# Kernel tuning notes

Measured on AMD Instinct MI355X. Metric: run time of the kernel, lower is better.

Reference implementation:

```python
import jax, jax.numpy as jnp
import numpy as np

H = 64        # hidden_dim
A = 21        # N_ACTIONS
B = 262144    # batch size


def setup_inputs() -> dict:
    key = jax.random.key(0)
    ks = jax.random.split(key, 32)

    def w(k, shape):
        fan_in = shape[0]
        return (jax.random.normal(k, shape, jnp.float32) / np.float32(np.sqrt(fan_in)))

    inp = {
        "x": jax.random.normal(ks[0], (B, 2, 2), jnp.float32),
        "b_act1": jax.random.randint(ks[1], (B,), 0, A),
        "b_act2": jax.random.randint(ks[2], (B,), 0, A),
        # enc: Linear(2,H), ReLU, Linear(H,H), ReLU
        "enc_w1": w(ks[3], (2, H)), "enc_b1": jnp.zeros((H,), jnp.float32),
        "enc_w2": w(ks[4], (H, H)), "enc_b2": jnp.zeros((H,), jnp.float32),
        # q_net: Linear(H,H), ReLU, Linear(H,A)
        "q_w1": w(ks[5], (H, H)), "q_b1": jnp.zeros((H,), jnp.float32),
        "q_w2": w(ks[6], (H, A)), "q_b2": jnp.zeros((A,), jnp.float32),
        # v_net: Linear(H,H), ReLU, Linear(H,1)
        "v_w1": w(ks[7], (H, H)), "v_b1": jnp.zeros((H,), jnp.float32),
        "v_w2": w(ks[8], (H, 1)), "v_b2": jnp.zeros((1,), jnp.float32),
        # lin2: Linear(H+A,H), ReLU, Linear(H,H), ReLU, Linear(H,H)
        "l2_w1": w(ks[9], (H + A, H)), "l2_b1": jnp.zeros((H,), jnp.float32),
        "l2_w2": w(ks[10], (H, H)), "l2_b2": jnp.zeros((H,), jnp.float32),
        "l2_w3": w(ks[11], (H, H)), "l2_b3": jnp.zeros((H,), jnp.float32),
        # lin3, lin4
        "l3_w": w(ks[12], (H, H)), "l3_b": jnp.zeros((H,), jnp.float32),
        "l4_w": w(ks[13], (H, A)), "l4_b": jnp.zeros((A,), jnp.float32),
        # q_prime_net: Linear(H,2H) ELU Linear(2H,H) ELU Linear(H,H) ELU Linear(H,1)
        "qp_w1": w(ks[14], (H, 2 * H)), "qp_b1": jnp.zeros((2 * H,), jnp.float32),
        "qp_w2": w(ks[15], (2 * H, H)), "qp_b2": jnp.zeros((H,), jnp.float32),
        "qp_w3": w(ks[16], (H, H)), "qp_b3": jnp.zeros((H,), jnp.float32),
        "qp_w4": w(ks[17], (H, 1)), "qp_b4": jnp.zeros((1,), jnp.float32),
    }
    return inp


def reference(x, b_act1, b_act2,
              enc_w1, enc_b1, enc_w2, enc_b2,
              q_w1, q_b1, q_w2, q_b2,
              v_w1, v_b1, v_w2, v_b2,
              l2_w1, l2_b1, l2_w2, l2_b2, l2_w3, l2_b3,
              l3_w, l3_b, l4_w, l4_b,
              qp_w1, qp_b1, qp_w2, qp_b2, qp_w3, qp_b3, qp_w4, qp_b4):
    relu = jax.nn.relu
    elu = jax.nn.elu

    def enc(z):
        return relu(relu(z @ enc_w1 + enc_b1) @ enc_w2 + enc_b2)

    def q_net(h):
        return relu(h @ q_w1 + q_b1) @ q_w2 + q_b2

    def lin2(e):  # ends with bare Linear (no final activation)
        h = relu(e @ l2_w1 + l2_b1)
        h = relu(h @ l2_w2 + l2_b2)
        return h @ l2_w3 + l2_b3

    def q_prime(z):
        h = elu(z @ qp_w1 + qp_b1)
        h = elu(h @ qp_w2 + qp_b2)
        h = elu(h @ qp_w3 + qp_b3)
        return h @ qp_w4 + qp_b4

    h1 = enc(x[:, 0, :])  # [B,H]
    h2 = enc(x[:, 1, :])
    q1, q2 = q_net(h1), q_net(h2)              # [B,A]
    key2 = jnp.stack([h1, h2], axis=1)          # [B,2,H]
    vtot = relu((h1 + h2) @ v_w1 + v_b1) @ v_w2 + v_b2  # [B,1]

    def joint(act1, act2):
        oh1 = jax.nn.one_hot(act1, A, dtype=h1.dtype)
        oh2 = jax.nn.one_hot(act2, A, dtype=h2.dtype)
        e = jnp.stack([jnp.concatenate([h1, oh1], axis=-1),
                       jnp.concatenate([h2, oh2], axis=-1)], axis=1)  # [B,2,H+A]
        key1 = lin2(e)                              # [B,2,H]
        q = q_prime(key1.mean(axis=1))              # [B,1]
        return key1, q

    key1, joint_qs = joint(b_act1, b_act2)
    a1_max = jnp.argmax(q1, axis=1)
    a2_max = jnp.argmax(q2, axis=1)
    key1_max, joint_max_qs = joint(a1_max, a2_max)

    def q_jt(k1):
        z = key2 + k1.mean(axis=1, keepdims=True) - k1 / 2  # [B,2,H]
        return relu(z @ l3_w + l3_b) @ l4_w + l4_b           # [B,2,A]

    q_jt_alt = q_jt(key1)
    q_jt_max_alt = q_jt(key1_max)

    return (q1, q2, joint_qs, joint_max_qs, vtot, q_jt_alt, q_jt_max_alt)
```

## Files before the change

kernel.cpp:

```cpp
#include <hip/hip_runtime.h>
#include <hip/hip_bf16.h>


#define B_TOT 262144

typedef __bf16 bf16_t;
typedef __bf16 bf16x4 __attribute__((ext_vector_type(4)));
typedef __bf16 bf16x8 __attribute__((ext_vector_type(8)));
typedef float  f32x2  __attribute__((ext_vector_type(2)));
typedef float  f32x4  __attribute__((ext_vector_type(4)));

#define MFMA16(a, b, c) __builtin_amdgcn_mfma_f32_16x16x32_bf16((a), (b), (c), 0, 0, 0)

enum : int {
  OFF_VW1  = 0,
  OFF_L2W1 = 4096,
  OFF_L2W2 = 8192,
  OFF_L2W3 = 12288,
  OFF_L3W  = 16384,
  OFF_L4W  = 20480,
  OFF_QP1  = 22528,
  OFF_QP2  = 30720,
  OFF_QP3  = 38912,
  WS_ELEMS = 43008
};
#define WS_BYTES (WS_ELEMS * 2)

enum : int {
  O_Q1   = 0,
  O_Q2   = 21 * B_TOT,
  O_JQ   = 42 * B_TOT,
  O_JMQ  = 43 * B_TOT,
  O_VT   = 44 * B_TOT,
  O_QJT  = 45 * B_TOT,
  O_QJTM = 87 * B_TOT
};

struct RDesc { const float* src; int K; int N; int NT; int off; };
struct RPack { RDesc d[9]; };

__global__ void repack_kernel(RPack P, bf16_t* __restrict__ ws) {
  RDesc d = P.d[blockIdx.x];
  int n = (d.K >> 5) * d.NT * 512;
  for (int i = threadIdx.x; i < n; i += blockDim.x) {
    int j  = i & 7;
    int l  = (i >> 3) & 63;
    int t  = i >> 9;
    int nt = t % d.NT;
    int kc = t / d.NT;
    int sk = kc * 32 + 16 * (j >> 2) + 4 * (l >> 4) + (j & 3);
    int sn = nt * 16 + (l & 15);
    float v = (sn < d.N) ? d.src[sk * d.N + sn] : 0.0f;
    ws[d.off + i] = (bf16_t)v;
  }
}

struct Args {
  const float* x; const int* a1; const int* a2;
  const float* ew1; const float* eb1; const float* ew2; const float* eb2;
  const float* qw1; const float* qb1; const float* qw2; const float* qb2;
  const float* vw1; const float* vb1; const float* vw2; const float* vb2;
  const float* l2w1; const float* l2b1; const float* l2w2; const float* l2b2;
  const float* l2w3; const float* l2b3;
  const float* l3w;  const float* l3b;  const float* l4w;  const float* l4b;
  const float* qpw1; const float* qpb1; const float* qpw2; const float* qpb2;
  const float* qpw3; const float* qpb3; const float* qpw4; const float* qpb4;
  float* out; const bf16_t* ws;
};

struct __align__(16) SMem {
  unsigned char scr[16896];
  bf16_t h1b[64 * 68];
  bf16_t h2b[64 * 68];
  float  bias[768];
  int    acts[128];
  int    amax[128];
  float  red[64][4];
  int    redi[64][4];
};

__device__ __forceinline__ float eluf(float x) {
  return x > 0.f ? x : __expf(x) - 1.0f;
}

__device__ __forceinline__ void fcA64ip(float* __restrict__ f,
                                        const float* __restrict__ W,
                                        const float* __restrict__ Bv,
                                        bf16_t* __restrict__ hb, int r, int g) {
  f32x2 acc[8];
  const f32x2* Bv2 = (const f32x2*)(Bv + g * 16);
#pragma unroll
  for (int i = 0; i < 8; i++) acc[i] = Bv2[i];
  const f32x2* fr = (const f32x2*)(f + r * 66);
#pragma unroll 1
  for (int hh = 0; hh < 2; hh++) {
    f32x2 in[16];
#pragma unroll
    for (int i = 0; i < 16; i++) in[i] = fr[16 * hh + i];
#pragma unroll 4
    for (int k2 = 0; k2 < 16; k2++) {
      int k = 32 * hh + 2 * k2;
      const f32x2* wr0 = (const f32x2*)(W + k * 64 + g * 16);
      const f32x2* wr1 = (const f32x2*)(W + (k + 1) * 64 + g * 16);
      f32x2 a0 = {in[k2][0], in[k2][0]};
      f32x2 a1 = {in[k2][1], in[k2][1]};
#pragma unroll
      for (int i = 0; i < 8; i++) acc[i] += a0 * wr0[i];
#pragma unroll
      for (int i = 0; i < 8; i++) acc[i] += a1 * wr1[i];
    }
  }
  __syncthreads();
#pragma unroll
  for (int i = 0; i < 8; i++) {
    float v0 = fmaxf(acc[i][0], 0.f), v1 = fmaxf(acc[i][1], 0.f);
    f32x2 v = {v0, v1};
    *(f32x2*)(f + r * 66 + g * 16 + 2 * i) = v;
    if (hb) {
      hb[r * 68 + g * 16 + 2 * i]     = (bf16_t)v0;
      hb[r * 68 + g * 16 + 2 * i + 1] = (bf16_t)v1;
    }
  }
  __syncthreads();
}

template <int NC>
__device__ __forceinline__ void qn2(const float* __restrict__ fin, const float* __restrict__ W21,
                                    const float* __restrict__ Bv, float* __restrict__ qo,
                                    int r, int colbase, float& bv, int& bi) {
  float acc[NC];
#pragma unroll
  for (int i = 0; i < NC; i++) acc[i] = Bv[colbase + i];
  for (int k2 = 0; k2 < 32; k2++) {
    f32x2 a = *(const f32x2*)(fin + r * 66 + 2 * k2);
    const float* wr0 = W21 + (2 * k2) * 21 + colbase;
    const float* wr1 = W21 + (2 * k2 + 1) * 21 + colbase;
#pragma unroll
    for (int i = 0; i < NC; i++) acc[i] = fmaf(a[0], wr0[i], acc[i]);
#pragma unroll
    for (int i = 0; i < NC; i++) acc[i] = fmaf(a[1], wr1[i], acc[i]);
  }
  bv = -3e38f; bi = 0;
#pragma unroll
  for (int i = 0; i < NC; i++) {
    qo[i] = acc[i];
    if (acc[i] > bv) { bv = acc[i]; bi = colbase + i; }
  }
}

template <bool USEWS, int NT, int KC>
__device__ __forceinline__ f32x4 tileT(const bf16x8* __restrict__ WF,
                                       const float* __restrict__ Wp, int N, int woff,
                                       const bf16x8* __restrict__ bin,
                                       const float* __restrict__ bias, int bbase,
                                       int nt, int l, int c, int u) {
  f32x4 a = *(const f32x4*)(bias + bbase + nt * 16 + 4 * u);
#pragma unroll
  for (int kc = 0; kc < KC; kc++) {
    bf16x8 w;
    if constexpr (USEWS) {
      w = WF[(woff >> 3) + (kc * NT + nt) * 64 + l];
    } else {
      int sn = nt * 16 + c;
      if (sn < N) {
#pragma unroll
        for (int j = 0; j < 8; j++)
          w[j] = (bf16_t)Wp[(kc * 32 + 16 * (j >> 2) + 4 * u + (j & 3)) * N + sn];
      } else {
#pragma unroll
        for (int j = 0; j < 8; j++) w[j] = (bf16_t)0.0f;
      }
    }
    a = MFMA16(w, bin[kc], a);
  }
  return a;
}

template <int MODE>
__device__ __forceinline__ bf16x8 pack2(f32x4 t0, f32x4 t1) {
  bf16x8 r;
#pragma unroll
  for (int j = 0; j < 8; j++) {
    float v = (j >> 2) ? t1[j & 3] : t0[j & 3];
    if constexpr (MODE == 1) v = fmaxf(v, 0.f);
    if constexpr (MODE == 2) v = eluf(v);
    r[j] = (bf16_t)v;
  }
  return r;
}

template <bool USEWS>
__global__ __launch_bounds__(256, 2) void qtran_main(Args A) {
  __shared__ SMem sm;
  const int t = threadIdx.x;
  const int wgbase = blockIdx.x * 64;
  const int r = t & 63;
  const int g = __builtin_amdgcn_readfirstlane(t >> 6);

  float* f0 = (float*)sm.scr;

  if (t < 64) {
    sm.bias[t]        = A.vb1[t];
    sm.bias[64 + t]   = A.l2b1[t];
    sm.bias[128 + t]  = A.l2b2[t];
    sm.bias[192 + t]  = A.l2b3[t];
    sm.bias[384 + t]  = A.qpb2[t];
    sm.bias[448 + t]  = A.qpb3[t];
    sm.bias[512 + t]  = A.l3b[t];
    sm.bias[608 + t]  = A.vw2[t];
    sm.bias[672 + t]  = A.qpw4[t];
    sm.acts[t]        = A.a1[wgbase + t];
    sm.acts[64 + t]   = A.a2[wgbase + t];
  } else if (t < 192) {
    sm.bias[256 + t - 64] = A.qpb1[t - 64];
  } else if (t < 224) {
    int i = t - 192;
    sm.bias[576 + i] = (i < 21) ? A.l4b[i] : 0.0f;
  } else if (t == 224) {
    sm.bias[736] = A.vb2[0];
    sm.bias[737] = A.qpb4[0];
  }

  const int rowg = wgbase + r;
  float4 xv = ((const float4*)A.x)[rowg];
#pragma unroll 1
  for (int s = 0; s < 2; ++s) {
    float xa = s ? xv.z : xv.x;
    float xb = s ? xv.w : xv.y;
#pragma unroll
    for (int cc = 0; cc < 16; cc += 2) {
      int col = g * 16 + cc;
      float h0 = fmaf(xa, A.ew1[col],     fmaf(xb, A.ew1[64 + col],     A.eb1[col]));
      float h1 = fmaf(xa, A.ew1[col + 1], fmaf(xb, A.ew1[64 + col + 1], A.eb1[col + 1]));
      f32x2 v = {fmaxf(h0, 0.f), fmaxf(h1, 0.f)};
      *(f32x2*)(f0 + r * 66 + col) = v;
    }
    __syncthreads();
    fcA64ip(f0, A.ew2, A.eb2, s ? sm.h2b : sm.h1b, r, g);
    fcA64ip(f0, A.qw1, A.qb1, nullptr, r, g);
    {
      float* qo = A.out + (s ? O_Q2 : O_Q1) + rowg * 21;
      float bv; int bi;
      if (g == 0)      qn2<6>(f0, A.qw2, A.qb2, qo,      r, 0,  bv, bi);
      else if (g == 1) qn2<5>(f0, A.qw2, A.qb2, qo + 6,  r, 6,  bv, bi);
      else if (g == 2) qn2<5>(f0, A.qw2, A.qb2, qo + 11, r, 11, bv, bi);
      else             qn2<5>(f0, A.qw2, A.qb2, qo + 16, r, 16, bv, bi);
      sm.red[r][g] = bv; sm.redi[r][g] = bi;
    }
    __syncthreads();
    if (t < 64) {
      float b0 = sm.red[t][0]; int i0 = sm.redi[t][0];
#pragma unroll
      for (int grp = 1; grp < 4; grp++)
        if (sm.red[t][grp] > b0) { b0 = sm.red[t][grp]; i0 = sm.redi[t][grp]; }
      sm.amax[s * 64 + t] = i0;
    }
    __syncthreads();
  }

  const int l = t & 63;
  const int c = l & 15, u = l >> 4;
  const int rb = g * 16;
  const int row = rb + c;
  float* out = A.out;
  const bf16x8* WF = (const bf16x8*)A.ws;
  const float* bias = sm.bias;
  float* S = (float*)sm.scr;

  auto HG = [&](const bf16_t* __restrict__ HB, int kc) -> bf16x8 {
    const bf16_t* p = HB + row * 68 + kc * 32 + 4 * u;
    bf16x4 lo = *(const bf16x4*)p;
    bf16x4 hi = *(const bf16x4*)(p + 16);
    bf16x8 rr;
#pragma unroll
    for (int d = 0; d < 4; d++) { rr[d] = lo[d]; rr[4 + d] = hi[d]; }
    return rr;
  };

  {
    bf16x8 aS[2];
#pragma unroll
    for (int kc = 0; kc < 2; kc++) {
      bf16x8 a1 = HG(sm.h1b, kc), a2 = HG(sm.h2b, kc);
      bf16x8 s8;
#pragma unroll
      for (int i = 0; i < 8; i++) s8[i] = (bf16_t)((float)a1[i] + (float)a2[i]);
      aS[kc] = s8;
    }
    float pr = 0.f;
#pragma unroll
    for (int nt = 0; nt < 4; nt++) {
      f32x4 tv = tileT<USEWS, 4, 2>(WF, A.vw1, 64, OFF_VW1, aS, bias, 0, nt, l, c, u);
      f32x4 wv = *(const f32x4*)(bias + 608 + nt * 16 + 4 * u);
#pragma unroll
      for (int p = 0; p < 4; p++) pr += fmaxf(tv[p], 0.f) * wv[p];
    }
    pr += __shfl_xor(pr, 16, 64);
    pr += __shfl_xor(pr, 32, 64);
    if (u == 0) out[O_VT + wgbase + row] = pr + bias[736];
  }

  auto J = [&](const int* __restrict__ asrc, int jointBase, int qjtBase) {
    bf16x8 k1f[2][2];
#pragma unroll
    for (int j = 0; j < 2; j++) {
      const bf16_t* HB = j ? sm.h2b : sm.h1b;
      const int act = asrc[j * 64 + row];
      bf16x8 bh[2];
#pragma unroll
      for (int kc = 0; kc < 2; kc++) bh[kc] = HG(HB, kc);
      const float* ohp = A.l2w1 + (64 + act) * 64 + 4 * u;
      bf16x8 b1[2];
#pragma unroll
      for (int f = 0; f < 2; f++) {
        f32x4 t0 = tileT<USEWS, 4, 2>(WF, A.l2w1, 64, OFF_L2W1, bh, bias, 64, 2 * f, l, c, u);
        f32x4 t1 = tileT<USEWS, 4, 2>(WF, A.l2w1, 64, OFF_L2W1, bh, bias, 64, 2 * f + 1, l, c, u);
        t0 += *(const f32x4*)(ohp + (2 * f) * 16);
        t1 += *(const f32x4*)(ohp + (2 * f + 1) * 16);
        b1[f] = pack2<1>(t0, t1);
      }
      bf16x8 b2[2];
#pragma unroll
      for (int f = 0; f < 2; f++) {
        f32x4 t0 = tileT<USEWS, 4, 2>(WF, A.l2w2, 64, OFF_L2W2, b1, bias, 128, 2 * f, l, c, u);
        f32x4 t1 = tileT<USEWS, 4, 2>(WF, A.l2w2, 64, OFF_L2W2, b1, bias, 128, 2 * f + 1, l, c, u);
        b2[f] = pack2<1>(t0, t1);
      }
#pragma unroll
      for (int f = 0; f < 2; f++) {
        f32x4 t0 = tileT<USEWS, 4, 2>(WF, A.l2w3, 64, OFF_L2W3, b2, bias, 192, 2 * f, l, c, u);
        f32x4 t1 = tileT<USEWS, 4, 2>(WF, A.l2w3, 64, OFF_L2W3, b2, bias, 192, 2 * f + 1, l, c, u);
        k1f[j][f] = pack2<0>(t0, t1);
      }
    }
#pragma unroll
    for (int j = 0; j < 2; j++) {
      const bf16_t* HB = j ? sm.h2b : sm.h1b;
      bf16x8 aZ[2];
#pragma unroll
      for (int kc = 0; kc < 2; kc++) {
        bf16x8 h8 = HG(HB, kc);
        bf16x8 kk = k1f[1 - j][kc];
#pragma unroll
        for (int i = 0; i < 8; i++)
          aZ[kc][i] = (bf16_t)((float)h8[i] + 0.5f * (float)kk[i]);
      }
      bf16x8 bz[2];
#pragma unroll
      for (int f = 0; f < 2; f++) {
        f32x4 t0 = tileT<USEWS, 4, 2>(WF, A.l3w, 64, OFF_L3W, aZ, bias, 512, 2 * f, l, c, u);
        f32x4 t1 = tileT<USEWS, 4, 2>(WF, A.l3w, 64, OFF_L3W, aZ, bias, 512, 2 * f + 1, l, c, u);
        bz[f] = pack2<1>(t0, t1);
      }
#pragma unroll
      for (int nt = 0; nt < 2; nt++) {
        f32x4 tq = tileT<USEWS, 2, 2>(WF, A.l4w, 21, OFF_L4W, bz, bias, 576, nt, l, c, u);
#pragma unroll
        for (int p = 0; p < 4; p++) {
          int n2 = nt * 16 + 4 * u + p;
          if (n2 < 21) S[row * 43 + j * 21 + n2] = tq[p];
        }
      }
    }
    bf16x8 aM[2];
#pragma unroll
    for (int kc = 0; kc < 2; kc++)
#pragma unroll
      for (int i = 0; i < 8; i++)
        aM[kc][i] = (bf16_t)(0.5f * ((float)k1f[0][kc][i] + (float)k1f[1][kc][i]));
    {
      const int ob = qjtBase + (wgbase + rb) * 42;
      const float* Sx = S + rb * 43;
      int colw = l, roww = 0;
      if (colw >= 42) { colw -= 42; roww = 1; }
      for (int i2 = l; i2 < 672; i2 += 64) {
        out[ob + i2] = Sx[roww * 43 + colw];
        colw += 22; roww += 1;
        if (colw >= 42) { colw -= 42; roww += 1; }
      }
    }
    bf16x8 bq[4];
#pragma unroll
    for (int f = 0; f < 4; f++) {
      f32x4 t0 = tileT<USEWS, 8, 2>(WF, A.qpw1, 128, OFF_QP1, aM, bias, 256, 2 * f, l, c, u);
      f32x4 t1 = tileT<USEWS, 8, 2>(WF, A.qpw1, 128, OFF_QP1, aM, bias, 256, 2 * f + 1, l, c, u);
      bq[f] = pack2<2>(t0, t1);
    }
    bf16x8 b3[2];
#pragma unroll
    for (int f = 0; f < 2; f++) {
      f32x4 t0 = tileT<USEWS, 4, 4>(WF, A.qpw2, 64, OFF_QP2, bq, bias, 384, 2 * f, l, c, u);
      f32x4 t1 = tileT<USEWS, 4, 4>(WF, A.qpw2, 64, OFF_QP2, bq, bias, 384, 2 * f + 1, l, c, u);
      b3[f] = pack2<2>(t0, t1);
    }
    float pj = 0.f;
#pragma unroll
    for (int nt = 0; nt < 4; nt++) {
      f32x4 tq = tileT<USEWS, 4, 2>(WF, A.qpw3, 64, OFF_QP3, b3, bias, 448, nt, l, c, u);
      f32x4 w4 = *(const f32x4*)(bias + 672 + nt * 16 + 4 * u);
#pragma unroll
      for (int p = 0; p < 4; p++) pj += eluf(tq[p]) * w4[p];
    }
    pj += __shfl_xor(pj, 16, 64);
    pj += __shfl_xor(pj, 32, 64);
    if (u == 0) out[jointBase + wgbase + row] = pj + bias[737];
  };

  J(sm.acts, O_JQ, O_QJT);
  J(sm.amax, O_JMQ, O_QJTM);
}

extern "C" void kernel_launch(void* const* d_in, const int* in_sizes, int n_in,
                              void* d_out, int out_size, void* d_ws, size_t ws_size,
                              hipStream_t stream) {
  (void)in_sizes; (void)n_in; (void)out_size;
  Args A;
  A.x    = (const float*)d_in[0];
  A.a1   = (const int*)d_in[1];
  A.a2   = (const int*)d_in[2];
  A.ew1  = (const float*)d_in[3];
  A.eb1  = (const float*)d_in[4];
  A.ew2  = (const float*)d_in[5];
  A.eb2  = (const float*)d_in[6];
  A.qw1  = (const float*)d_in[7];
  A.qb1  = (const float*)d_in[8];
  A.qw2  = (const float*)d_in[9];
  A.qb2  = (const float*)d_in[10];
  A.vw1  = (const float*)d_in[11];
  A.vb1  = (const float*)d_in[12];
  A.vw2  = (const float*)d_in[13];
  A.vb2  = (const float*)d_in[14];
  A.l2w1 = (const float*)d_in[15];
  A.l2b1 = (const float*)d_in[16];
  A.l2w2 = (const float*)d_in[17];
  A.l2b2 = (const float*)d_in[18];
  A.l2w3 = (const float*)d_in[19];
  A.l2b3 = (const float*)d_in[20];
  A.l3w  = (const float*)d_in[21];
  A.l3b  = (const float*)d_in[22];
  A.l4w  = (const float*)d_in[23];
  A.l4b  = (const float*)d_in[24];
  A.qpw1 = (const float*)d_in[25];
  A.qpb1 = (const float*)d_in[26];
  A.qpw2 = (const float*)d_in[27];
  A.qpb2 = (const float*)d_in[28];
  A.qpw3 = (const float*)d_in[29];
  A.qpb3 = (const float*)d_in[30];
  A.qpw4 = (const float*)d_in[31];
  A.qpb4 = (const float*)d_in[32];
  A.out  = (float*)d_out;
  A.ws   = (const bf16_t*)d_ws;

  if (ws_size >= (size_t)WS_BYTES) {
    bf16_t* ws = (bf16_t*)d_ws;
    RPack P;
    P.d[0] = {A.vw1,  64, 64,  4, OFF_VW1};
    P.d[1] = {A.l2w1, 64, 64,  4, OFF_L2W1};
    P.d[2] = {A.l2w2, 64, 64,  4, OFF_L2W2};
    P.d[3] = {A.l2w3, 64, 64,  4, OFF_L2W3};
    P.d[4] = {A.l3w,  64, 64,  4, OFF_L3W};
    P.d[5] = {A.l4w,  64, 21,  2, OFF_L4W};
    P.d[6] = {A.qpw1, 64, 128, 8, OFF_QP1};
    P.d[7] = {A.qpw2, 128, 64, 4, OFF_QP2};
    P.d[8] = {A.qpw3, 64, 64,  4, OFF_QP3};
    hipLaunchKernelGGL(repack_kernel, dim3(9), dim3(256), 0, stream, P, ws);
    hipLaunchKernelGGL(HIP_KERNEL_NAME(qtran_main<true>), dim3(B_TOT / 64), dim3(256), 0,
                       stream, A);
  } else {
    hipLaunchKernelGGL(HIP_KERNEL_NAME(qtran_main<false>), dim3(B_TOT / 64), dim3(256), 0,
                       stream, A);
  }
}
```

Measured before the change: 903.0 us.

## Prefetch weight fragments into registers and double-buffer them across MLP layers

Splits the weight-fragment load out of the MFMA tile helper so each layer's weights are loaded into register arrays once and reused for both tokens (h1/h2) instead of being re-fetched per token. The lin2 layers now process both tokens together, and the next layer's weights are loaded into an alternate buffer while the current layer's MFMAs run, hiding global/L2 load latency. This raises register pressure (two 8-entry bf16x8 buffers plus more live activations), which under launch_bounds(256,2) could cause spills.

```diff
diff --git a/kernel.cpp b/kernel.cpp
--- a/kernel.cpp
+++ b/kernel.cpp
@@ -148,31 +148,41 @@
   }
 }
 
-template <bool USEWS, int NT, int KC>
-__device__ __forceinline__ f32x4 tileT(const bf16x8* __restrict__ WF,
-                                       const float* __restrict__ Wp, int N, int woff,
-                                       const bf16x8* __restrict__ bin,
-                                       const float* __restrict__ bias, int bbase,
-                                       int nt, int l, int c, int u) {
-  f32x4 a = *(const f32x4*)(bias + bbase + nt * 16 + 4 * u);
-#pragma unroll
-  for (int kc = 0; kc < KC; kc++) {
-    bf16x8 w;
-    if constexpr (USEWS) {
-      w = WF[(woff >> 3) + (kc * NT + nt) * 64 + l];
-    } else {
-      int sn = nt * 16 + c;
-      if (sn < N) {
-#pragma unroll
-        for (int j = 0; j < 8; j++)
-          w[j] = (bf16_t)Wp[(kc * 32 + 16 * (j >> 2) + 4 * u + (j & 3)) * N + sn];
+template <bool USEWS, int NT, int KC, int NT0, int NTN>
+__device__ __forceinline__ void loadW(const bf16x8* __restrict__ WF,
+                                      const float* __restrict__ Wp, int N, int woff,
+                                      int l, int c, int u, bf16x8* __restrict__ w) {
+#pragma unroll
+  for (int kc = 0; kc < KC; kc++)
+#pragma unroll
+    for (int i = 0; i < NTN; i++) {
+      const int nt = NT0 + i;
+      if constexpr (USEWS) {
+        w[kc * NTN + i] = WF[(woff >> 3) + (kc * NT + nt) * 64 + l];
       } else {
-#pragma unroll
-        for (int j = 0; j < 8; j++) w[j] = (bf16_t)0.0f;
+        const int sn = nt * 16 + c;
+        bf16x8 v;
+        if (sn < N) {
+#pragma unroll
+          for (int j = 0; j < 8; j++)
+            v[j] = (bf16_t)Wp[(kc * 32 + 16 * (j >> 2) + 4 * u + (j & 3)) * N + sn];
+        } else {
+#pragma unroll
+          for (int j = 0; j < 8; j++) v[j] = (bf16_t)0.0f;
+        }
+        w[kc * NTN + i] = v;
       }
     }
-    a = MFMA16(w, bin[kc], a);
-  }
+}
+
+template <int KC, int NTN>
+__device__ __forceinline__ f32x4 mmaT(const bf16x8* __restrict__ w,
+                                      const bf16x8* __restrict__ bin,
+                                      const float* __restrict__ bias, int bbase,
+                                      int ntAbs, int i, int u) {
+  f32x4 a = *(const f32x4*)(bias + bbase + ntAbs * 16 + 4 * u);
+#pragma unroll
+  for (int kc = 0; kc < KC; kc++) a = MFMA16(w[kc * NTN + i], bin[kc], a);
   return a;
 }
 
@@ -278,6 +288,8 @@
   };
 
   {
+    bf16x8 wv[8];
+    loadW<USEWS, 4, 2, 0, 4>(WF, A.vw1, 64, OFF_VW1, l, c, u, wv);
     bf16x8 aS[2];
 #pragma unroll
     for (int kc = 0; kc < 2; kc++) {
@@ -290,10 +302,10 @@
     float pr = 0.f;
 #pragma unroll
     for (int nt = 0; nt < 4; nt++) {
-      f32x4 tv = tileT<USEWS, 4, 2>(WF, A.vw1, 64, OFF_VW1, aS, bias, 0, nt, l, c, u);
-      f32x4 wv = *(const f32x4*)(bias + 608 + nt * 16 + 4 * u);
-#pragma unroll
-      for (int p = 0; p < 4; p++) pr += fmaxf(tv[p], 0.f) * wv[p];
+      f32x4 tv = mmaT<2, 4>(wv, aS, bias, 0, nt, nt, u);
+      f32x4 wvv = *(const f32x4*)(bias + 608 + nt * 16 + 4 * u);
+#pragma unroll
+      for (int p = 0; p < 4; p++) pr += fmaxf(tv[p], 0.f) * wvv[p];
     }
     pr += __shfl_xor(pr, 16, 64);
     pr += __shfl_xor(pr, 32, 64);
@@ -301,67 +313,84 @@
   }
 
   auto J = [&](const int* __restrict__ asrc, int jointBase, int qjtBase) {
+    bf16x8 wA[8], wB[8];
+    bf16x8 bh[2][2];
+#pragma unroll
+    for (int j = 0; j < 2; j++)
+#pragma unroll
+      for (int kc = 0; kc < 2; kc++) bh[j][kc] = HG(j ? sm.h2b : sm.h1b, kc);
+    const int act0 = asrc[row], act1 = asrc[64 + row];
+    f32x4 oh[2][4];
+#pragma unroll
+    for (int f = 0; f < 4; f++) {
+      oh[0][f] = *(const f32x4*)(A.l2w1 + (64 + act0) * 64 + 4 * u + f * 16);
+      oh[1][f] = *(const f32x4*)(A.l2w1 + (64 + act1) * 64 + 4 * u + f * 16);
+    }
+    loadW<USEWS, 4, 2, 0, 4>(WF, A.l2w1, 64, OFF_L2W1, l, c, u, wA);
+    loadW<USEWS, 4, 2, 0, 4>(WF, A.l2w2, 64, OFF_L2W2, l, c, u, wB);
+    bf16x8 b1[2][2];
+#pragma unroll
+    for (int j = 0; j < 2; j++) {
+      f32x4 t0 = mmaT<2, 4>(wA, bh[j], bias, 64, 0, 0, u); t0 += oh[j][0];
+      f32x4 t1 = mmaT<2, 4>(wA, bh[j], bias, 64, 1, 1, u); t1 += oh[j][1];
+      f32x4 t2 = mmaT<2, 4>(wA, bh[j], bias, 64, 2, 2, u); t2 += oh[j][2];
+      f32x4 t3 = mmaT<2, 4>(wA, bh[j], bias, 64, 3, 3, u); t3 += oh[j][3];
+      b1[j][0] = pack2<1>(t0, t1);
+      b1[j][1] = pack2<1>(t2, t3);
+    }
+    loadW<USEWS, 4, 2, 0, 4>(WF, A.l2w3, 64, OFF_L2W3, l, c, u, wA);
+    bf16x8 b2[2][2];
+#pragma unroll
+    for (int j = 0; j < 2; j++) {
+      f32x4 t0 = mmaT<2, 4>(wB, b1[j], bias, 128, 0, 0, u);
+      f32x4 t1 = mmaT<2, 4>(wB, b1[j], bias, 128, 1, 1, u);
+      f32x4 t2 = mmaT<2, 4>(wB, b1[j], bias, 128, 2, 2, u);
+      f32x4 t3 = mmaT<2, 4>(wB, b1[j], bias, 128, 3, 3, u);
+      b2[j][0] = pack2<1>(t0, t1);
+      b2[j][1] = pack2<1>(t2, t3);
+    }
+    loadW<USEWS, 4, 2, 0, 4>(WF, A.l3w, 64, OFF_L3W, l, c, u, wB);
     bf16x8 k1f[2][2];
 #pragma unroll
     for (int j = 0; j < 2; j++) {
-      const bf16_t* HB = j ? sm.h2b : sm.h1b;
-      const int act = asrc[j * 64 + row];
-      bf16x8 bh[2];
-#pragma unroll
-      for (int kc = 0; kc < 2; kc++) bh[kc] = HG(HB, kc);
-      const float* ohp = A.l2w1 + (64 + act) * 64 + 4 * u;
-      bf16x8 b1[2];
-#pragma unroll
-      for (int f = 0; f < 2; f++) {
-        f32x4 t0 = tileT<USEWS, 4, 2>(WF, A.l2w1, 64, OFF_L2W1, bh, bias, 64, 2 * f, l, c, u);
-        f32x4 t1 = tileT<USEWS, 4, 2>(WF, A.l2w1, 64, OFF_L2W1, bh, bias, 64, 2 * f + 1, l, c, u);
-        t0 += *(const f32x4*)(ohp + (2 * f) * 16);
-        t1 += *(const f32x4*)(ohp + (2 * f + 1) * 16);
-        b1[f] = pack2<1>(t0, t1);
+      f32x4 t0 = mmaT<2, 4>(wA, b2[j], bias, 192, 0, 0, u);
+      f32x4 t1 = mmaT<2, 4>(wA, b2[j], bias, 192, 1, 1, u);
+      f32x4 t2 = mmaT<2, 4>(wA, b2[j], bias, 192, 2, 2, u);
+      f32x4 t3 = mmaT<2, 4>(wA, b2[j], bias, 192, 3, 3, u);
+      k1f[j][0] = pack2<0>(t0, t1);
+      k1f[j][1] = pack2<0>(t2, t3);
+    }
+    loadW<USEWS, 2, 2, 0, 2>(WF, A.l4w, 21, OFF_L4W, l, c, u, wA);
+    bf16x8 bz[2][2];
+#pragma unroll
+    for (int j = 0; j < 2; j++) {
+      bf16x8 aZ[2];
+#pragma unroll
+      for (int kc = 0; kc < 2; kc++) {
+        bf16x8 kk = k1f[1 - j][kc];
+#pragma unroll
+        for (int i = 0; i < 8; i++)
+          aZ[kc][i] = (bf16_t)((float)bh[j][kc][i] + 0.5f * (float)kk[i]);
       }
-      bf16x8 b2[2];
-#pragma unroll
-      for (int f = 0; f < 2; f++) {
-        f32x4 t0 = tileT<USEWS, 4, 2>(WF, A.l2w2, 64, OFF_L2W2, b1, bias, 128, 2 * f, l, c, u);
-        f32x4 t1 = tileT<USEWS, 4, 2>(WF, A.l2w2, 64, OFF_L2W2, b1, bias, 128, 2 * f + 1, l, c, u);
-        b2[f] = pack2<1>(t0, t1);
-      }
-#pragma unroll
-      for (int f = 0; f < 2; f++) {
-        f32x4 t0 = tileT<USEWS, 4, 2>(WF, A.l2w3, 64, OFF_L2W3, b2, bias, 192, 2 * f, l, c, u);
-        f32x4 t1 = tileT<USEWS, 4, 2>(WF, A.l2w3, 64, OFF_L2W3, b2, bias, 192, 2 * f + 1, l, c, u);
-        k1f[j][f] = pack2<0>(t0, t1);
-      }
-    }
-#pragma unroll
-    for (int j = 0; j < 2; j++) {
-      const bf16_t* HB = j ? sm.h2b : sm.h1b;
-      bf16x8 aZ[2];
-#pragma unroll
-      for (int kc = 0; kc < 2; kc++) {
-        bf16x8 h8 = HG(HB, kc);
-        bf16x8 kk = k1f[1 - j][kc];
-#pragma unroll
-        for (int i = 0; i < 8; i++)
-          aZ[kc][i] = (bf16_t)((float)h8[i] + 0.5f * (float)kk[i]);
-      }
-      bf16x8 bz[2];
-#pragma unroll
-      for (int f = 0; f < 2; f++) {
-        f32x4 t0 = tileT<USEWS, 4, 2>(WF, A.l3w, 64, OFF_L3W, aZ, bias, 512, 2 * f, l, c, u);
-        f32x4 t1 = tileT<USEWS, 4, 2>(WF, A.l3w, 64, OFF_L3W, aZ, bias, 512, 2 * f + 1, l, c, u);
-        bz[f] = pack2<1>(t0, t1);
-      }
+      f32x4 t0 = mmaT<2, 4>(wB, aZ, bias, 512, 0, 0, u);
+      f32x4 t1 = mmaT<2, 4>(wB, aZ, bias, 512, 1, 1, u);
+      f32x4 t2 = mmaT<2, 4>(wB, aZ, bias, 512, 2, 2, u);
+      f32x4 t3 = mmaT<2, 4>(wB, aZ, bias, 512, 3, 3, u);
+      bz[j][0] = pack2<1>(t0, t1);
+      bz[j][1] = pack2<1>(t2, t3);
+    }
+    loadW<USEWS, 8, 2, 0, 4>(WF, A.qpw1, 128, OFF_QP1, l, c, u, wB);
+#pragma unroll
+    for (int j = 0; j < 2; j++)
 #pragma unroll
       for (int nt = 0; nt < 2; nt++) {
-        f32x4 tq = tileT<USEWS, 2, 2>(WF, A.l4w, 21, OFF_L4W, bz, bias, 576, nt, l, c, u);
+        f32x4 tq = mmaT<2, 2>(wA, bz[j], bias, 576, nt, nt, u);
 #pragma unroll
         for (int p = 0; p < 4; p++) {
           int n2 = nt * 16 + 4 * u + p;
           if (n2 < 21) S[row * 43 + j * 21 + n2] = tq[p];
         }
       }
-    }
     bf16x8 aM[2];
 #pragma unroll
     for (int kc = 0; kc < 2; kc++)
@@ -379,24 +408,42 @@
         if (colw >= 42) { colw -= 42; roww += 1; }
       }
     }
+    loadW<USEWS, 8, 2, 4, 4>(WF, A.qpw1, 128, OFF_QP1, l, c, u, wA);
     bf16x8 bq[4];
-#pragma unroll
-    for (int f = 0; f < 4; f++) {
-      f32x4 t0 = tileT<USEWS, 8, 2>(WF, A.qpw1, 128, OFF_QP1, aM, bias, 256, 2 * f, l, c, u);
-      f32x4 t1 = tileT<USEWS, 8, 2>(WF, A.qpw1, 128, OFF_QP1, aM, bias, 256, 2 * f + 1, l, c, u);
-      bq[f] = pack2<2>(t0, t1);
-    }
+    {
+      f32x4 t0 = mmaT<2, 4>(wB, aM, bias, 256, 0, 0, u);
+      f32x4 t1 = mmaT<2, 4>(wB, aM, bias, 256, 1, 1, u);
+      f32x4 t2 = mmaT<2, 4>(wB, aM, bias, 256, 2, 2, u);
+      f32x4 t3 = mmaT<2, 4>(wB, aM, bias, 256, 3, 3, u);
+      bq[0] = pack2<2>(t0, t1);
+      bq[1] = pack2<2>(t2, t3);
+    }
+    loadW<USEWS, 4, 4, 0, 2>(WF, A.qpw2, 64, OFF_QP2, l, c, u, wB);
+    {
+      f32x4 t0 = mmaT<2, 4>(wA, aM, bias, 256, 4, 0, u);
+      f32x4 t1 = mmaT<2, 4>(wA, aM, bias, 256, 5, 1, u);
+      f32x4 t2 = mmaT<2, 4>(wA, aM, bias, 256, 6, 2, u);
+      f32x4 t3 = mmaT<2, 4>(wA, aM, bias, 256, 7, 3, u);
+      bq[2] = pack2<2>(t0, t1);
+      bq[3] = pack2<2>(t2, t3);
+    }
+    loadW<USEWS, 4, 4, 2, 2>(WF, A.qpw2, 64, OFF_QP2, l, c, u, wA);
     bf16x8 b3[2];
-#pragma unroll
-    for (int f = 0; f < 2; f++) {
-      f32x4 t0 = tileT<USEWS, 4, 4>(WF, A.qpw2, 64, OFF_QP2, bq, bias, 384, 2 * f, l, c, u);
-      f32x4 t1 = tileT<USEWS, 4, 4>(WF, A.qpw2, 64, OFF_QP2, bq, bias, 384, 2 * f + 1, l, c, u);
-      b3[f] = pack2<2>(t0, t1);
+    {
+      f32x4 t0 = mmaT<4, 2>(wB, bq, bias, 384, 0, 0, u);
+      f32x4 t1 = mmaT<4, 2>(wB, bq, bias, 384, 1, 1, u);
+      b3[0] = pack2<2>(t0, t1);
+    }
+    loadW<USEWS, 4, 2, 0, 4>(WF, A.qpw3, 64, OFF_QP3, l, c, u, wB);
+    {
+      f32x4 t0 = mmaT<4, 2>(wA, bq, bias, 384, 2, 0, u);
+      f32x4 t1 = mmaT<4, 2>(wA, bq, bias, 384, 3, 1, u);
+      b3[1] = pack2<2>(t0, t1);
     }
     float pj = 0.f;
 #pragma unroll
     for (int nt = 0; nt < 4; nt++) {
-      f32x4 tq = tileT<USEWS, 4, 2>(WF, A.qpw3, 64, OFF_QP3, b3, bias, 448, nt, l, c, u);
+      f32x4 tq = mmaT<2, 4>(wB, b3, bias, 448, nt, nt, u);
       f32x4 w4 = *(const f32x4*)(bias + 672 + nt * 16 + 4 * u);
 #pragma unroll
       for (int p = 0; p < 4; p++) pj += eluf(tq[p]) * w4[p];
```

Measured after the change: 901.5 us. No clear change (-0.2%).

## Split fused kernel into encoder/q-net kernel and joint kernel via output scratch

Applied to the files above, without the earlier changes.

The single fused kernel is split into two launches. The first computes the encoders, q_net and argmax with a smaller LDS footprint and higher launch-bound occupancy. It stashes bf16 hidden states and argmax indices into not-yet-written regions of the output buffer. The second kernel reloads them and runs the MFMA-based joint/qprime/q_jt stages with its own occupancy target. This trades extra global round-trips and a launch for better per-stage occupancy and register budgets.

```diff
diff --git a/kernel.cpp b/kernel.cpp
--- a/kernel.cpp
+++ b/kernel.cpp
@@ -68,20 +68,18 @@
   float* out; const bf16_t* ws;
 };
 
-struct __align__(16) SMem {
-  unsigned char scr[16896];
-  bf16_t h1b[64 * 68];
-  bf16_t h2b[64 * 68];
-  float  bias[768];
-  int    acts[128];
-  int    amax[128];
+__device__ __forceinline__ float eluf(float x) {
+  return x > 0.f ? x : __expf(x) - 1.0f;
+}
+
+
+struct __align__(16) SMemA {
+  float  f0[64 * 66];
+  bf16_t h1[64 * 64];
+  bf16_t h2[64 * 64];
   float  red[64][4];
   int    redi[64][4];
 };
-
-__device__ __forceinline__ float eluf(float x) {
-  return x > 0.f ? x : __expf(x) - 1.0f;
-}
 
 __device__ __forceinline__ void fcA64ip(float* __restrict__ f,
                                         const float* __restrict__ W,
@@ -117,8 +115,8 @@
     f32x2 v = {v0, v1};
     *(f32x2*)(f + r * 66 + g * 16 + 2 * i) = v;
     if (hb) {
-      hb[r * 68 + g * 16 + 2 * i]     = (bf16_t)v0;
-      hb[r * 68 + g * 16 + 2 * i + 1] = (bf16_t)v1;
+      hb[r * 64 + g * 16 + 2 * i]     = (bf16_t)v0;
+      hb[r * 64 + g * 16 + 2 * i + 1] = (bf16_t)v1;
     }
   }
   __syncthreads();
@@ -147,6 +145,71 @@
     if (acc[i] > bv) { bv = acc[i]; bi = colbase + i; }
   }
 }
+
+__global__ __launch_bounds__(256, 4) void qtran_a(Args A) {
+  __shared__ SMemA sm;
+  const int t = threadIdx.x;
+  const int wgbase = blockIdx.x * 64;
+  const int r = t & 63;
+  const int g = __builtin_amdgcn_readfirstlane(t >> 6);
+  float* f0 = sm.f0;
+  float* out = A.out;
+
+  const int rowg = wgbase + r;
+  float4 xv = ((const float4*)A.x)[rowg];
+#pragma unroll 1
+  for (int s = 0; s < 2; ++s) {
+    float xa = s ? xv.z : xv.x;
+    float xb = s ? xv.w : xv.y;
+#pragma unroll
+    for (int cc = 0; cc < 16; cc += 2) {
+      int col = g * 16 + cc;
+      float h0 = fmaf(xa, A.ew1[col],     fmaf(xb, A.ew1[64 + col],     A.eb1[col]));
+      float h1 = fmaf(xa, A.ew1[col + 1], fmaf(xb, A.ew1[64 + col + 1], A.eb1[col + 1]));
+      f32x2 v = {fmaxf(h0, 0.f), fmaxf(h1, 0.f)};
+      *(f32x2*)(f0 + r * 66 + col) = v;
+    }
+    __syncthreads();
+    fcA64ip(f0, A.ew2, A.eb2, s ? sm.h2 : sm.h1, r, g);
+    fcA64ip(f0, A.qw1, A.qb1, nullptr, r, g);
+    {
+      float* qo = out + (s ? O_Q2 : O_Q1) + rowg * 21;
+      float bv; int bi;
+      if (g == 0)      qn2<6>(f0, A.qw2, A.qb2, qo,      r, 0,  bv, bi);
+      else if (g == 1) qn2<5>(f0, A.qw2, A.qb2, qo + 6,  r, 6,  bv, bi);
+      else if (g == 2) qn2<5>(f0, A.qw2, A.qb2, qo + 11, r, 11, bv, bi);
+      else             qn2<5>(f0, A.qw2, A.qb2, qo + 16, r, 16, bv, bi);
+      sm.red[r][g] = bv; sm.redi[r][g] = bi;
+    }
+    __syncthreads();
+    if (t < 64) {
+      float b0 = sm.red[t][0]; int i0 = sm.redi[t][0];
+#pragma unroll
+      for (int grp = 1; grp < 4; grp++)
+        if (sm.red[t][grp] > b0) { b0 = sm.red[t][grp]; i0 = sm.redi[t][grp]; }
+      out[(s ? O_JMQ : O_JQ) + wgbase + t] = __int_as_float(i0);
+    }
+    __syncthreads();
+  }
+
+  const uint* h1w = (const uint*)sm.h1;
+  const uint* h2w = (const uint*)sm.h2;
+  for (int i = t; i < 2048; i += 256) {
+    int row = i >> 5, w = i & 31;
+    out[O_QJT  + (wgbase + row) * 42 + w] = __uint_as_float(h1w[row * 32 + w]);
+    out[O_QJTM + (wgbase + row) * 42 + w] = __uint_as_float(h2w[row * 32 + w]);
+  }
+}
+
+
+struct __align__(16) SMemB {
+  float  S[64 * 43];
+  bf16_t h1b[64 * 68];
+  bf16_t h2b[64 * 68];
+  float  bias[768];
+  int    acts[128];
+  int    amax[128];
+};
 
 template <bool USEWS, int NT, int KC>
 __device__ __forceinline__ f32x4 tileT(const bf16x8* __restrict__ WF,
@@ -190,14 +253,11 @@
 }
 
 template <bool USEWS>
-__global__ __launch_bounds__(256, 2) void qtran_main(Args A) {
-  __shared__ SMem sm;
+__global__ __launch_bounds__(256, 3) void qtran_b(Args A) {
+  __shared__ SMemB sm;
   const int t = threadIdx.x;
   const int wgbase = blockIdx.x * 64;
-  const int r = t & 63;
-  const int g = __builtin_amdgcn_readfirstlane(t >> 6);
-
-  float* f0 = (float*)sm.scr;
+  float* out = A.out;
 
   if (t < 64) {
     sm.bias[t]        = A.vb1[t];
@@ -211,6 +271,8 @@
     sm.bias[672 + t]  = A.qpw4[t];
     sm.acts[t]        = A.a1[wgbase + t];
     sm.acts[64 + t]   = A.a2[wgbase + t];
+    sm.amax[t]        = __float_as_int(out[O_JQ + wgbase + t]);
+    sm.amax[64 + t]   = __float_as_int(out[O_JMQ + wgbase + t]);
   } else if (t < 192) {
     sm.bias[256 + t - 64] = A.qpb1[t - 64];
   } else if (t < 224) {
@@ -220,52 +282,25 @@
     sm.bias[736] = A.vb2[0];
     sm.bias[737] = A.qpb4[0];
   }
-
-  const int rowg = wgbase + r;
-  float4 xv = ((const float4*)A.x)[rowg];
-#pragma unroll 1
-  for (int s = 0; s < 2; ++s) {
-    float xa = s ? xv.z : xv.x;
-    float xb = s ? xv.w : xv.y;
-#pragma unroll
-    for (int cc = 0; cc < 16; cc += 2) {
-      int col = g * 16 + cc;
-      float h0 = fmaf(xa, A.ew1[col],     fmaf(xb, A.ew1[64 + col],     A.eb1[col]));
-      float h1 = fmaf(xa, A.ew1[col + 1], fmaf(xb, A.ew1[64 + col + 1], A.eb1[col + 1]));
-      f32x2 v = {fmaxf(h0, 0.f), fmaxf(h1, 0.f)};
-      *(f32x2*)(f0 + r * 66 + col) = v;
-    }
-    __syncthreads();
-    fcA64ip(f0, A.ew2, A.eb2, s ? sm.h2b : sm.h1b, r, g);
-    fcA64ip(f0, A.qw1, A.qb1, nullptr, r, g);
-    {
-      float* qo = A.out + (s ? O_Q2 : O_Q1) + rowg * 21;
-      float bv; int bi;
-      if (g == 0)      qn2<6>(f0, A.qw2, A.qb2, qo,      r, 0,  bv, bi);
-      else if (g == 1) qn2<5>(f0, A.qw2, A.qb2, qo + 6,  r, 6,  bv, bi);
-      else if (g == 2) qn2<5>(f0, A.qw2, A.qb2, qo + 11, r, 11, bv, bi);
-      else             qn2<5>(f0, A.qw2, A.qb2, qo + 16, r, 16, bv, bi);
-      sm.red[r][g] = bv; sm.redi[r][g] = bi;
-    }
-    __syncthreads();
-    if (t < 64) {
-      float b0 = sm.red[t][0]; int i0 = sm.redi[t][0];
-#pragma unroll
-      for (int grp = 1; grp < 4; grp++)
-        if (sm.red[t][grp] > b0) { b0 = sm.red[t][grp]; i0 = sm.redi[t][grp]; }
-      sm.amax[s * 64 + t] = i0;
-    }
-    __syncthreads();
-  }
+  {
+    uint* h1w = (uint*)sm.h1b;
+    uint* h2w = (uint*)sm.h2b;
+    for (int i = t; i < 2048; i += 256) {
+      int row = i >> 5, w = i & 31;
+      h1w[row * 34 + w] = __float_as_uint(out[O_QJT  + (wgbase + row) * 42 + w]);
+      h2w[row * 34 + w] = __float_as_uint(out[O_QJTM + (wgbase + row) * 42 + w]);
+    }
+  }
+  __syncthreads();
 
   const int l = t & 63;
   const int c = l & 15, u = l >> 4;
+  const int g = __builtin_amdgcn_readfirstlane(t >> 6);
   const int rb = g * 16;
   const int row = rb + c;
-  float* out = A.out;
   const bf16x8* WF = (const bf16x8*)A.ws;
   const float* bias = sm.bias;
-  float* S = (float*)sm.scr;
+  float* S = sm.S;
 
   auto HG = [&](const bf16_t* __restrict__ HB, int kc) -> bf16x8 {
     const bf16_t* p = HB + row * 68 + kc * 32 + 4 * u;
@@ -451,6 +486,8 @@
   A.out  = (float*)d_out;
   A.ws   = (const bf16_t*)d_ws;
 
+  hipLaunchKernelGGL(qtran_a, dim3(B_TOT / 64), dim3(256), 0, stream, A);
+
   if (ws_size >= (size_t)WS_BYTES) {
     bf16_t* ws = (bf16_t*)d_ws;
     RPack P;
@@ -464,10 +501,10 @@
     P.d[7] = {A.qpw2, 128, 64, 4, OFF_QP2};
     P.d[8] = {A.qpw3, 64, 64,  4, OFF_QP3};
     hipLaunchKernelGGL(repack_kernel, dim3(9), dim3(256), 0, stream, P, ws);
-    hipLaunchKernelGGL(HIP_KERNEL_NAME(qtran_main<true>), dim3(B_TOT / 64), dim3(256), 0,
+    hipLaunchKernelGGL(HIP_KERNEL_NAME(qtran_b<true>), dim3(B_TOT / 64), dim3(256), 0,
                        stream, A);
   } else {
-    hipLaunchKernelGGL(HIP_KERNEL_NAME(qtran_main<false>), dim3(B_TOT / 64), dim3(256), 0,
+    hipLaunchKernelGGL(HIP_KERNEL_NAME(qtran_b<false>), dim3(B_TOT / 64), dim3(256), 0,
                        stream, A);
   }
 }
```

Measured after the change: 921.5 us. 1.02x slower.
